# Kernel tuning notes

Hardware: AMD Instinct MI355X
Metric: run time of the kernel (lower is better)

The kernel has to match this reference:

```python
import jax, jax.numpy as jnp
import numpy as np

D_MODEL = 256
NUM_HEADS = 4
HEAD_DIM = D_MODEL // NUM_HEADS
B, N, M = 1, 768, 768


def setup_inputs() -> dict:
    key = jax.random.key(0)
    ks = jax.random.split(key, 12)
    s = 1.0 / np.sqrt(D_MODEL)
    inp = {
        "input_q": jax.random.normal(ks[0], (B, N, D_MODEL), jnp.float32),
        "input_k": jax.random.normal(ks[1], (B, M, D_MODEL), jnp.float32),
        "input_v": jax.random.normal(ks[2], (B, M, D_MODEL), jnp.float32),
        "embed_qk": jax.random.normal(ks[3], (B, N, M, D_MODEL), jnp.float32),
        "Wq": jax.random.normal(ks[4], (D_MODEL, D_MODEL), jnp.float32) * s,
        "bq": jax.random.normal(ks[5], (D_MODEL,), jnp.float32) * s,
        "Wk": jax.random.normal(ks[6], (D_MODEL, D_MODEL), jnp.float32) * s,
        "bk": jax.random.normal(ks[7], (D_MODEL,), jnp.float32) * s,
        "Wv": jax.random.normal(ks[8], (D_MODEL, D_MODEL), jnp.float32) * s,
        "bv": jax.random.normal(ks[9], (D_MODEL,), jnp.float32) * s,
        "Wp": jax.random.normal(ks[10], (D_MODEL, D_MODEL), jnp.float32) * s,
        "bp": jax.random.normal(ks[11], (D_MODEL,), jnp.float32) * s,
    }
    return inp


def _split_heads(x):
    # (b, n, h*c) -> (b, h, n, c)
    b, n, _ = x.shape
    return x.reshape(b, n, NUM_HEADS, HEAD_DIM).transpose(0, 2, 1, 3)


def reference(input_q, input_k, input_v, embed_qk, Wq, bq, Wk, bk, Wv, bv, Wp, bp):
    q = _split_heads(input_q @ Wq.T + bq)                      # (b,h,n,c)
    k = _split_heads(input_k @ Wk.T + bk)                      # (b,h,m,c)
    v = _split_heads(input_v @ Wv.T + bv)                      # (b,h,m,c)
    p = embed_qk @ Wp.T + bp                                   # (b,n,m,h*c)
    p = p.reshape(B, N, M, NUM_HEADS, HEAD_DIM).transpose(0, 3, 1, 2, 4)  # (b,h,n,m,c)

    scores_p = jnp.einsum('bhnc,bhnmc->bhnm', q, p)
    scores_e = jnp.einsum('bhnc,bhmc->bhnm', q, k)
    scores = (scores_e + scores_p) / jnp.sqrt(jnp.float32(HEAD_DIM))
    attn = jax.nn.softmax(scores, axis=-1)                     # (b,h,n,m)
    hidden = jnp.einsum('bhnm,bhmc->bhnc', attn, v)
    hidden = hidden.transpose(0, 2, 1, 3).reshape(B, N, D_MODEL)  # (b,n,h*c)
    return hidden, attn
```

## Files before the change

kernel.cpp:

```cpp
#include <hip/hip_runtime.h>

#define DM    256
#define NHD   4
#define HD    64
#define NSEQ  768
#define MSEQ  768

#define WS_Q  0
#define WS_K  196608
#define WS_V  393216
#define WS_U  589824

typedef float nativef4 __attribute__((ext_vector_type(4)));

template<int CTRL, bool BC>
static __device__ __forceinline__ float dpp_mov_f(float x) {
    int xi = __float_as_int(x);
    int r = __builtin_amdgcn_update_dpp(BC ? 0 : xi, xi, CTRL, 0xF, 0xF, BC);
    return __int_as_float(r);
}
static __device__ __forceinline__ float row16_sum(float x) {
    x += dpp_mov_f<0x111, true>(x);
    x += dpp_mov_f<0x112, true>(x);
    x += dpp_mov_f<0x114, true>(x);
    x += dpp_mov_f<0x118, true>(x);
    return x;
}
static __device__ __forceinline__ float wave_sum(float x) {
    x = row16_sum(x);
    x += dpp_mov_f<0x142, true>(x);
    x += dpp_mov_f<0x143, true>(x);
    return x;
}
static __device__ __forceinline__ float wave_max(float x) {
    x = fmaxf(x, dpp_mov_f<0x111, false>(x));
    x = fmaxf(x, dpp_mov_f<0x112, false>(x));
    x = fmaxf(x, dpp_mov_f<0x114, false>(x));
    x = fmaxf(x, dpp_mov_f<0x118, false>(x));
    x = fmaxf(x, dpp_mov_f<0x142, false>(x));
    x = fmaxf(x, dpp_mov_f<0x143, false>(x));
    return x;
}

__global__ __launch_bounds__(256) void proj_nt_kernel(
    const float* __restrict__ Xq, const float* __restrict__ Xk, const float* __restrict__ Xv,
    const float* __restrict__ Wq, const float* __restrict__ Wk, const float* __restrict__ Wv,
    const float* __restrict__ bq, const float* __restrict__ bk, const float* __restrict__ bv,
    float* __restrict__ ws)
{
    const int z = blockIdx.z;
    const float* X    = (z == 0) ? Xq : (z == 1) ? Xk : Xv;
    const float* W    = (z == 0) ? Wq : (z == 1) ? Wk : Wv;
    const float* bias = (z == 0) ? bq : (z == 1) ? bk : bv;
    float* C = ws + (size_t)z * (NSEQ * DM);

    const int n0 = blockIdx.x * 64;
    const int j0 = blockIdx.y * 64;
    const int t  = threadIdx.x;
    const int ar  = t & 63;
    const int seg = (t >> 6) << 4;
    const int tr  = t >> 4;
    const int tc  = t & 15;

    __shared__ float Al[64 * 68];
    __shared__ float Bl[64 * 68];

    float acc[4][4] = {};

    for (int kc = 0; kc < 4; ++kc) {
        const int k0 = kc * 64;
        {
            const float4* s4 = (const float4*)(X + (size_t)(n0 + ar) * DM + k0 + seg);
            float tmp[16];
            *(float4*)&tmp[0]  = s4[0]; *(float4*)&tmp[4]  = s4[1];
            *(float4*)&tmp[8]  = s4[2]; *(float4*)&tmp[12] = s4[3];
            #pragma unroll
            for (int w2 = 0; w2 < 16; ++w2) Al[(seg + w2) * 68 + ar] = tmp[w2];
        }
        {
            const float4* s4 = (const float4*)(W + (size_t)(j0 + ar) * DM + k0 + seg);
            float tmp[16];
            *(float4*)&tmp[0]  = s4[0]; *(float4*)&tmp[4]  = s4[1];
            *(float4*)&tmp[8]  = s4[2]; *(float4*)&tmp[12] = s4[3];
            #pragma unroll
            for (int w2 = 0; w2 < 16; ++w2) Bl[(seg + w2) * 68 + ar] = tmp[w2];
        }
        __syncthreads();
        #pragma unroll 8
        for (int kk = 0; kk < 64; ++kk) {
            float4 a = *(const float4*)&Al[kk * 68 + tr * 4];
            float4 b = *(const float4*)&Bl[kk * 68 + tc * 4];
            acc[0][0] = fmaf(a.x, b.x, acc[0][0]); acc[0][1] = fmaf(a.x, b.y, acc[0][1]);
            acc[0][2] = fmaf(a.x, b.z, acc[0][2]); acc[0][3] = fmaf(a.x, b.w, acc[0][3]);
            acc[1][0] = fmaf(a.y, b.x, acc[1][0]); acc[1][1] = fmaf(a.y, b.y, acc[1][1]);
            acc[1][2] = fmaf(a.y, b.z, acc[1][2]); acc[1][3] = fmaf(a.y, b.w, acc[1][3]);
            acc[2][0] = fmaf(a.z, b.x, acc[2][0]); acc[2][1] = fmaf(a.z, b.y, acc[2][1]);
            acc[2][2] = fmaf(a.z, b.z, acc[2][2]); acc[2][3] = fmaf(a.z, b.w, acc[2][3]);
            acc[3][0] = fmaf(a.w, b.x, acc[3][0]); acc[3][1] = fmaf(a.w, b.y, acc[3][1]);
            acc[3][2] = fmaf(a.w, b.z, acc[3][2]); acc[3][3] = fmaf(a.w, b.w, acc[3][3]);
        }
        __syncthreads();
    }

    const float b0 = bias[j0 + tc * 4 + 0];
    const float b1 = bias[j0 + tc * 4 + 1];
    const float b2 = bias[j0 + tc * 4 + 2];
    const float b3 = bias[j0 + tc * 4 + 3];
    #pragma unroll
    for (int i = 0; i < 4; ++i) {
        float4 o;
        o.x = acc[i][0] + b0; o.y = acc[i][1] + b1;
        o.z = acc[i][2] + b2; o.w = acc[i][3] + b3;
        *(float4*)(C + (size_t)(n0 + tr * 4 + i) * DM + j0 + tc * 4) = o;
    }
}

__global__ __launch_bounds__(256) void u_nn_kernel(
    const float* __restrict__ qproj, const float* __restrict__ Wp, float* __restrict__ U)
{
    const int h  = blockIdx.z;
    const int n0 = blockIdx.x * 64;
    const int d0 = blockIdx.y * 64;
    const int t  = threadIdx.x;

    __shared__ float Al[64 * 68];
    __shared__ float Bl[64 * 68];

    {
        const int ar = t & 63, seg = (t >> 6) << 4;
        const float4* s4 = (const float4*)(qproj + (size_t)(n0 + ar) * DM + h * HD + seg);
        float tmp[16];
        *(float4*)&tmp[0]  = s4[0]; *(float4*)&tmp[4]  = s4[1];
        *(float4*)&tmp[8]  = s4[2]; *(float4*)&tmp[12] = s4[3];
        #pragma unroll
        for (int w2 = 0; w2 < 16; ++w2) Al[(seg + w2) * 68 + ar] = tmp[w2];
    }
    {
        const int c = t >> 2, dseg = (t & 3) << 4;
        const float4* s4 = (const float4*)(Wp + (size_t)(h * HD + c) * DM + d0 + dseg);
        float4 v0 = s4[0], v1 = s4[1], v2 = s4[2], v3 = s4[3];
        *(float4*)&Bl[c * 68 + dseg + 0]  = v0;
        *(float4*)&Bl[c * 68 + dseg + 4]  = v1;
        *(float4*)&Bl[c * 68 + dseg + 8]  = v2;
        *(float4*)&Bl[c * 68 + dseg + 12] = v3;
    }
    __syncthreads();

    const int tr = t >> 4, tc = t & 15;
    float acc[4][4] = {};
    #pragma unroll 8
    for (int kk = 0; kk < 64; ++kk) {
        float4 a = *(const float4*)&Al[kk * 68 + tr * 4];
        float4 b = *(const float4*)&Bl[kk * 68 + tc * 4];
        acc[0][0] = fmaf(a.x, b.x, acc[0][0]); acc[0][1] = fmaf(a.x, b.y, acc[0][1]);
        acc[0][2] = fmaf(a.x, b.z, acc[0][2]); acc[0][3] = fmaf(a.x, b.w, acc[0][3]);
        acc[1][0] = fmaf(a.y, b.x, acc[1][0]); acc[1][1] = fmaf(a.y, b.y, acc[1][1]);
        acc[1][2] = fmaf(a.y, b.z, acc[1][2]); acc[1][3] = fmaf(a.y, b.w, acc[1][3]);
        acc[2][0] = fmaf(a.z, b.x, acc[2][0]); acc[2][1] = fmaf(a.z, b.y, acc[2][1]);
        acc[2][2] = fmaf(a.z, b.z, acc[2][2]); acc[2][3] = fmaf(a.z, b.w, acc[2][3]);
        acc[3][0] = fmaf(a.w, b.x, acc[3][0]); acc[3][1] = fmaf(a.w, b.y, acc[3][1]);
        acc[3][2] = fmaf(a.w, b.z, acc[3][2]); acc[3][3] = fmaf(a.w, b.w, acc[3][3]);
    }

    #pragma unroll
    for (int i = 0; i < 4; ++i) {
        float4 o; o.x = acc[i][0]; o.y = acc[i][1]; o.z = acc[i][2]; o.w = acc[i][3];
        *(float4*)(U + (size_t)(n0 + tr * 4 + i) * (NHD * DM) + h * DM + d0 + tc * 4) = o;
    }
}

__global__ __launch_bounds__(768, 6) void attn_main_kernel(
    const float* __restrict__ embed, const float* __restrict__ ws, float* __restrict__ out)
{
    const float* qproj = ws + WS_Q;
    const float* kproj = ws + WS_K;
    const float* vproj = ws + WS_V;
    const float* U     = ws + WS_U;

    const int n    = blockIdx.x;
    const int tid  = threadIdx.x;
    const int wid  = tid >> 6;
    const int lane = tid & 63;

    __shared__ float sc[4 * 776];
    __shared__ float part[12 * 256];
    __shared__ float redm[12], reds[12];

    {
        const int h   = lane >> 4;
        const int c16 = (lane & 15) << 4;
        const int c4  = (lane & 15) << 2;

        const float4* uP = (const float4*)(U + (size_t)n * (NHD * DM) + h * DM + c16);
        const float4 U0 = uP[0], U1 = uP[1], U2 = uP[2], U3 = uP[3];
        const float4 Q4 = *(const float4*)(qproj + (size_t)n * DM + h * HD + c4);

        const size_t ebase = (size_t)n * MSEQ * DM;
        #pragma unroll 2
        for (int i = 0; i < 64; ++i) {
            const int m = wid * 64 + i;
            const nativef4* e4 = (const nativef4*)(embed + ebase + (size_t)m * DM + c16);
            nativef4 e0 = __builtin_nontemporal_load(e4 + 0);
            nativef4 e1 = __builtin_nontemporal_load(e4 + 1);
            nativef4 e2 = __builtin_nontemporal_load(e4 + 2);
            nativef4 e3 = __builtin_nontemporal_load(e4 + 3);
            float4 K4 = *(const float4*)(kproj + (size_t)m * DM + h * HD + c4);

            float pa = fmaf(e0.x, U0.x, fmaf(e0.y, U0.y, fmaf(e0.z, U0.z, e0.w * U0.w)));
            float pb = fmaf(e1.x, U1.x, fmaf(e1.y, U1.y, fmaf(e1.z, U1.z, e1.w * U1.w)));
            float pc = fmaf(e2.x, U2.x, fmaf(e2.y, U2.y, fmaf(e2.z, U2.z, e2.w * U2.w)));
            float pd = fmaf(e3.x, U3.x, fmaf(e3.y, U3.y, fmaf(e3.z, U3.z, e3.w * U3.w)));
            float pe = fmaf(K4.x, Q4.x, fmaf(K4.y, Q4.y, fmaf(K4.z, Q4.z, K4.w * Q4.w)));
            float p = ((pa + pb) + (pc + pd)) + pe;
            p = row16_sum(p);
            if ((lane & 15) == 15) sc[h * 776 + m] = p;
        }
    }
    __syncthreads();

    {
        const int h = wid & 3, third = wid >> 2;
        const int mm = third * 256 + (lane << 2);
        float4 p4 = *(const float4*)&sc[h * 776 + mm];
        const float v0 = p4.x * 0.125f, v1 = p4.y * 0.125f;
        const float v2 = p4.z * 0.125f, v3 = p4.w * 0.125f;

        float wmax = wave_max(fmaxf(fmaxf(v0, v1), fmaxf(v2, v3)));
        if (lane == 63) redm[wid] = wmax;
        __syncthreads();
        const float rmax = fmaxf(fmaxf(redm[h], redm[h + 4]), redm[h + 8]);

        const float x0 = __expf(v0 - rmax), x1 = __expf(v1 - rmax);
        const float x2 = __expf(v2 - rmax), x3 = __expf(v3 - rmax);
        float wsum = wave_sum((x0 + x1) + (x2 + x3));
        if (lane == 63) reds[wid] = wsum;
        __syncthreads();
        const float inv = 1.0f / (reds[h] + reds[h + 4] + reds[h + 8]);

        float4 a4;
        a4.x = x0 * inv; a4.y = x1 * inv; a4.z = x2 * inv; a4.w = x3 * inv;
        *(float4*)&sc[h * 776 + mm] = a4;

        nativef4 an = { a4.x, a4.y, a4.z, a4.w };
        float* aout = out + (size_t)NSEQ * DM + ((size_t)h * NSEQ + n) * MSEQ + mm;
        __builtin_nontemporal_store(an, (nativef4*)aout);
    }
    __syncthreads();

    {
        const int g  = tid >> 6;
        const int jb = (tid & 63) << 2;
        const int h  = jb >> 6;
        const int mbase = g * 64;
        float4 acc = make_float4(0.f, 0.f, 0.f, 0.f);
        for (int mi = 0; mi < 64; mi += 4) {
            float4 a4 = *(const float4*)&sc[h * 776 + mbase + mi];
            float4 va = *(const float4*)(vproj + (size_t)(mbase + mi + 0) * DM + jb);
            float4 vb = *(const float4*)(vproj + (size_t)(mbase + mi + 1) * DM + jb);
            float4 vc = *(const float4*)(vproj + (size_t)(mbase + mi + 2) * DM + jb);
            float4 vd = *(const float4*)(vproj + (size_t)(mbase + mi + 3) * DM + jb);
            acc.x = fmaf(a4.x, va.x, acc.x); acc.y = fmaf(a4.x, va.y, acc.y);
            acc.z = fmaf(a4.x, va.z, acc.z); acc.w = fmaf(a4.x, va.w, acc.w);
            acc.x = fmaf(a4.y, vb.x, acc.x); acc.y = fmaf(a4.y, vb.y, acc.y);
            acc.z = fmaf(a4.y, vb.z, acc.z); acc.w = fmaf(a4.y, vb.w, acc.w);
            acc.x = fmaf(a4.z, vc.x, acc.x); acc.y = fmaf(a4.z, vc.y, acc.y);
            acc.z = fmaf(a4.z, vc.z, acc.z); acc.w = fmaf(a4.z, vc.w, acc.w);
            acc.x = fmaf(a4.w, vd.x, acc.x); acc.y = fmaf(a4.w, vd.y, acc.y);
            acc.z = fmaf(a4.w, vd.z, acc.z); acc.w = fmaf(a4.w, vd.w, acc.w);
        }
        *(float4*)&part[g * 256 + jb] = acc;
    }
    __syncthreads();
    if (tid < 256) {
        float s = 0.f;
        #pragma unroll
        for (int g = 0; g < 12; ++g) s += part[g * 256 + tid];
        out[(size_t)n * DM + tid] = s;
    }
}

extern "C" void kernel_launch(void* const* d_in, const int* in_sizes, int n_in,
                              void* d_out, int out_size, void* d_ws, size_t ws_size,
                              hipStream_t stream) {
    const float* input_q = (const float*)d_in[0];
    const float* input_k = (const float*)d_in[1];
    const float* input_v = (const float*)d_in[2];
    const float* embed   = (const float*)d_in[3];
    const float* Wq      = (const float*)d_in[4];
    const float* bq      = (const float*)d_in[5];
    const float* Wk      = (const float*)d_in[6];
    const float* bk      = (const float*)d_in[7];
    const float* Wv      = (const float*)d_in[8];
    const float* bv      = (const float*)d_in[9];
    const float* Wp      = (const float*)d_in[10];

    float* ws  = (float*)d_ws;
    float* out = (float*)d_out;

    dim3 g1(12, 4, 3);
    proj_nt_kernel<<<g1, 256, 0, stream>>>(input_q, input_k, input_v,
                                           Wq, Wk, Wv, bq, bk, bv, ws);
    dim3 g2(12, 4, 4);
    u_nn_kernel<<<g2, 256, 0, stream>>>(ws + WS_Q, Wp, ws + WS_U);

    attn_main_kernel<<<768, 768, 0, stream>>>(embed, ws, out);
}
```

Baseline: 906.0 us.

## Remap embed-score loop so each lane covers all heads over contiguous columns

Changes the phase-1 work split so each lane loads one float4 of the embed row, with the whole wave covering the 256 contiguous columns in a single coalesced load. The dot products against all four head projection vectors U0..U3 are computed per lane, then reduced with four full-wave sums instead of one 16-lane sum. The aim is better coalescing of the dominant embed stream and more loads in flight through deeper unrolling, at the cost of four wave-wide reductions per row instead of one.

```diff
diff --git a/kernel.cpp b/kernel.cpp
--- a/kernel.cpp
+++ b/kernel.cpp
@@ -187,33 +187,43 @@
     __shared__ float redm[12], reds[12];
 
     {
-        const int h   = lane >> 4;
-        const int c16 = (lane & 15) << 4;
-        const int c4  = (lane & 15) << 2;
-
-        const float4* uP = (const float4*)(U + (size_t)n * (NHD * DM) + h * DM + c16);
-        const float4 U0 = uP[0], U1 = uP[1], U2 = uP[2], U3 = uP[3];
-        const float4 Q4 = *(const float4*)(qproj + (size_t)n * DM + h * HD + c4);
-
-        const size_t ebase = (size_t)n * MSEQ * DM;
-        #pragma unroll 2
+        const int c4 = lane << 2;
+        const int hl = lane >> 4;
+
+        const float* Ub = U + (size_t)n * (NHD * DM);
+        const float4 U0 = *(const float4*)(Ub + 0 * DM + c4);
+        const float4 U1 = *(const float4*)(Ub + 1 * DM + c4);
+        const float4 U2 = *(const float4*)(Ub + 2 * DM + c4);
+        const float4 U3 = *(const float4*)(Ub + 3 * DM + c4);
+        const float4 Q4 = *(const float4*)(qproj + (size_t)n * DM + c4);
+
+        const size_t ebase = (size_t)n * MSEQ * DM + c4;
+        #pragma unroll 4
         for (int i = 0; i < 64; ++i) {
             const int m = wid * 64 + i;
-            const nativef4* e4 = (const nativef4*)(embed + ebase + (size_t)m * DM + c16);
-            nativef4 e0 = __builtin_nontemporal_load(e4 + 0);
-            nativef4 e1 = __builtin_nontemporal_load(e4 + 1);
-            nativef4 e2 = __builtin_nontemporal_load(e4 + 2);
-            nativef4 e3 = __builtin_nontemporal_load(e4 + 3);
-            float4 K4 = *(const float4*)(kproj + (size_t)m * DM + h * HD + c4);
-
-            float pa = fmaf(e0.x, U0.x, fmaf(e0.y, U0.y, fmaf(e0.z, U0.z, e0.w * U0.w)));
-            float pb = fmaf(e1.x, U1.x, fmaf(e1.y, U1.y, fmaf(e1.z, U1.z, e1.w * U1.w)));
-            float pc = fmaf(e2.x, U2.x, fmaf(e2.y, U2.y, fmaf(e2.z, U2.z, e2.w * U2.w)));
-            float pd = fmaf(e3.x, U3.x, fmaf(e3.y, U3.y, fmaf(e3.z, U3.z, e3.w * U3.w)));
-            float pe = fmaf(K4.x, Q4.x, fmaf(K4.y, Q4.y, fmaf(K4.z, Q4.z, K4.w * Q4.w)));
-            float p = ((pa + pb) + (pc + pd)) + pe;
-            p = row16_sum(p);
-            if ((lane & 15) == 15) sc[h * 776 + m] = p;
+            nativef4 e = __builtin_nontemporal_load(
+                (const nativef4*)(embed + ebase + (size_t)m * DM));
+            float4 K4 = *(const float4*)(kproj + (size_t)m * DM + c4);
+
+            float p0 = fmaf(e.x, U0.x, fmaf(e.y, U0.y, fmaf(e.z, U0.z, e.w * U0.w)));
+            float p1 = fmaf(e.x, U1.x, fmaf(e.y, U1.y, fmaf(e.z, U1.z, e.w * U1.w)));
+            float p2 = fmaf(e.x, U2.x, fmaf(e.y, U2.y, fmaf(e.z, U2.z, e.w * U2.w)));
+            float p3 = fmaf(e.x, U3.x, fmaf(e.y, U3.y, fmaf(e.z, U3.z, e.w * U3.w)));
+            float pk = fmaf(K4.x, Q4.x, fmaf(K4.y, Q4.y, fmaf(K4.z, Q4.z, K4.w * Q4.w)));
+            p0 += (hl == 0) ? pk : 0.0f;
+            p1 += (hl == 1) ? pk : 0.0f;
+            p2 += (hl == 2) ? pk : 0.0f;
+            p3 += (hl == 3) ? pk : 0.0f;
+            p0 = wave_sum(p0);
+            p1 = wave_sum(p1);
+            p2 = wave_sum(p2);
+            p3 = wave_sum(p3);
+            if (lane == 63) {
+                sc[0 * 776 + m] = p0;
+                sc[1 * 776 + m] = p1;
+                sc[2 * 776 + m] = p2;
+                sc[3 * 776 + m] = p3;
+            }
         }
     }
     __syncthreads();
```

Result: faster. 828.9 us (-8.5%).
